# Performance work log

Measured on AMD Instinct MI355X. Metric: run time of the kernel, lower is better.

The kernel has to match this reference:

```python
import jax, jax.numpy as jnp
import numpy as np

N = 2_000_000
FUN, TAU, ALPHA, LOSS_WEIGHT = 'log', 1.0, 1.0, 1.0


def setup_inputs() -> dict:
    key = jax.random.key(0)
    k1, k2, k3 = jax.random.split(key, 3)
    pred = jax.random.uniform(k1, (N, 5), dtype=jnp.float32)
    target = jax.random.uniform(k2, (N, 5), dtype=jnp.float32)
    weight = jax.random.uniform(k3, (N,), dtype=jnp.float32)
    return {"pred": pred, "target": target, "weight": weight}


def _xyrs(xywhr):
    # [N,5] -> xy [N,2], R [N,2,2], S [N,2,2] (diag(wh/2))
    xy = xywhr[:, :2]
    wh = xywhr[:, 2:4]
    r = xywhr[:, 4]
    c, s = jnp.cos(r), jnp.sin(r)
    R = jnp.stack([c, -s, s, c], axis=-1).reshape(-1, 2, 2)
    S = 0.5 * wh[:, :, None] * jnp.eye(2, dtype=xywhr.dtype)  # diag_embed
    return xy, R, S


def _sqrt_trace_2x2sym(M):
    # trace of matrix sqrt of symmetric PSD 2x2: sqrt(tr(M) + 2*sqrt(det(M)))
    a, b, d = M[:, 0, 0], M[:, 0, 1], M[:, 1, 1]
    det = jnp.clip(a * d - b * b, 0.0)
    return jnp.sqrt(jnp.clip(a + d + 2.0 * jnp.sqrt(det), 0.0))


def reference(pred, target, weight):
    xy_p, R_p, S_p = _xyrs(pred)
    xy_t, R_t, S_t = _xyrs(target)

    dxy = xy_p - xy_t
    xy_distance = jnp.sum(dxy * dxy, axis=-1)

    Rp_T = jnp.swapaxes(R_p, -1, -2)
    Rt_T = jnp.swapaxes(R_t, -1, -2)
    Sigma_p_sqrt = R_p @ S_p @ Rp_T
    Sigma_p = R_p @ (S_p * S_p) @ Rp_T
    Sigma_t = R_t @ (S_t * S_t) @ Rt_T

    whr_distance = Sigma_p[:, 0, 0] + Sigma_p[:, 1, 1]
    whr_distance = whr_distance + Sigma_t[:, 0, 0] + Sigma_t[:, 1, 1]
    cross = Sigma_p_sqrt @ Sigma_t @ Sigma_p_sqrt
    whr_distance = whr_distance - 2.0 * _sqrt_trace_2x2sym(cross)

    distance = jnp.sqrt(jnp.clip(xy_distance + ALPHA * whr_distance, 0.0))
    scale = jnp.sqrt(jnp.sqrt(jnp.prod(pred[:, 2:4] * target[:, 2:4], axis=-1)))
    distance = distance / scale

    if FUN == 'log':
        distance = jnp.log1p(distance)
    elif FUN == 'sqrt':
        distance = jnp.sqrt(distance)

    if TAU >= 1.0:
        loss = 1.0 - 1.0 / (TAU + distance)
    else:
        loss = distance

    # weighted_loss wrapper: elementwise weight then mean reduction
    loss = jnp.mean(loss * weight)
    return loss * LOSS_WEIGHT
```

## Files before the change

### kernel.cpp

```cpp
#include <hip/hip_runtime.h>


#define CHUNK_ROWS 1024

__device__ __forceinline__ float gwd_row(const float* __restrict__ p,
                                         const float* __restrict__ t)
{
    const float px = p[0], py = p[1], pw = p[2], ph = p[3], pr = p[4];
    const float tx = t[0], ty = t[1], tw = t[2], th = t[3], tr = t[4];

    const float dx = px - tx;
    const float dy = py - ty;
    const float xy_dist = dx * dx + dy * dy;

    const float a2p = 0.25f * pw * pw;
    const float b2p = 0.25f * ph * ph;
    const float a2t = 0.25f * tw * tw;
    const float b2t = 0.25f * th * th;

    float whr = (a2p + b2p) + (a2t + b2t);

    float cp, sp, ct, st;
    __sincosf(pr, &sp, &cp);
    __sincosf(tr, &st, &ct);

    const float Sp00 = cp * cp * a2p + sp * sp * b2p;
    const float Sp01 = cp * sp * (a2p - b2p);
    const float Sp11 = sp * sp * a2p + cp * cp * b2p;
    const float St00 = ct * ct * a2t + st * st * b2t;
    const float St01 = ct * st * (a2t - b2t);
    const float St11 = st * st * a2t + ct * ct * b2t;

    const float tr_cross  = Sp00 * St00 + 2.0f * Sp01 * St01 + Sp11 * St11;
    const float det_cross = (a2p * b2p) * (a2t * b2t);

    float sq = fmaxf(tr_cross + 2.0f * sqrtf(det_cross), 0.0f);
    whr = whr - 2.0f * sqrtf(sq);

    float distance = sqrtf(fmaxf(xy_dist + whr, 0.0f));

    const float prod = (pw * tw) * (ph * th);
    distance = distance / sqrtf(sqrtf(prod));

    distance = log1pf(distance);
    return 1.0f - 1.0f / (1.0f + distance);
}

__global__ __launch_bounds__(256) void gwd_loss_kernel(
    const float* __restrict__ pred,
    const float* __restrict__ target,
    const float* __restrict__ weight,
    float* __restrict__ out,
    int n)
{
    __shared__ float s_pred[CHUNK_ROWS * 5];
    __shared__ float s_tgt [CHUNK_ROWS * 5];

    const float inv_n = 1.0f / (float)n;
    const int row0 = blockIdx.x * CHUNK_ROWS;
    const int tid  = threadIdx.x;
    float acc = 0.0f;

    if (row0 + CHUNK_ROWS <= n) {
        const float4* p4 = (const float4*)(pred   + (size_t)row0 * 5);
        const float4* t4 = (const float4*)(target + (size_t)row0 * 5);

        float4 P[5], T[5];
        #pragma unroll
        for (int j = 0; j < 5; ++j) P[j] = p4[j * 256 + tid];
        #pragma unroll
        for (int j = 0; j < 5; ++j) T[j] = t4[j * 256 + tid];

        #pragma unroll
        for (int j = 0; j < 5; ++j) ((float4*)s_pred)[j * 256 + tid] = P[j];
        #pragma unroll
        for (int j = 0; j < 5; ++j) ((float4*)s_tgt )[j * 256 + tid] = T[j];
        __syncthreads();

        #pragma unroll
        for (int rr = 0; rr < 4; ++rr) {
            const int r = tid + rr * 256;
            acc += gwd_row(&s_pred[r * 5], &s_tgt[r * 5]) * weight[row0 + r];
        }
    } else {
        for (int r = row0 + tid; r < n; r += 256) {
            float pb[5], tb[5];
            #pragma unroll
            for (int k = 0; k < 5; ++k) {
                pb[k] = pred  [(size_t)r * 5 + k];
                tb[k] = target[(size_t)r * 5 + k];
            }
            acc += gwd_row(pb, tb) * weight[r];
        }
    }

    #pragma unroll
    for (int off = 32; off > 0; off >>= 1)
        acc += __shfl_down(acc, off, 64);

    __syncthreads();
    const int lane = tid & 63;
    const int wid  = tid >> 6;
    if (lane == 0) s_pred[wid] = acc;
    __syncthreads();

    if (tid == 0) {
        const float s = (s_pred[0] + s_pred[1]) + (s_pred[2] + s_pred[3]);
        atomicAdd(out, s * inv_n);
    }
}

extern "C" void kernel_launch(void* const* d_in, const int* in_sizes, int n_in,
                              void* d_out, int out_size, void* d_ws, size_t ws_size,
                              hipStream_t stream) {
    const float* pred   = (const float*)d_in[0];
    const float* target = (const float*)d_in[1];
    const float* weight = (const float*)d_in[2];
    float* out = (float*)d_out;

    const int n = in_sizes[2];

    hipMemsetAsync(out, 0, sizeof(float), stream);

    const int block = 256;
    const int grid  = (n + CHUNK_ROWS - 1) / CHUNK_ROWS;
    gwd_loss_kernel<<<grid, block, 0, stream>>>(pred, target, weight, out, n);
}
```

Before: 125.2 us.

## Use grid-stride per-thread float4 loads, two-pass reduction, fast math intrinsics

Replaces the LDS-staged chunk kernel with a fixed 1024-block grid-stride kernel. Each thread loads four contiguous rows as five float4s from pred and target plus one float4 of weights directly into registers. Per-block partial sums are written to the workspace and combined by a second single-block kernel that also handles the tail rows. This drops the memset and global atomics. Math is switched to raw hardware sqrt, rsq, log and rcp intrinsics, which reduces accuracy slightly. Per-thread strided float4 loads are less coalesced than the previous layout, and the extra launch adds fixed overhead.

```diff
diff --git a/kernel.cpp b/kernel.cpp
--- a/kernel.cpp
+++ b/kernel.cpp
@@ -1,7 +1,7 @@
 #include <hip/hip_runtime.h>
 
 
-#define CHUNK_ROWS 1024
+#define NBLK 1024
 
 __device__ __forceinline__ float gwd_row(const float* __restrict__ p,
                                          const float* __restrict__ t)
@@ -34,79 +34,105 @@
     const float tr_cross  = Sp00 * St00 + 2.0f * Sp01 * St01 + Sp11 * St11;
     const float det_cross = (a2p * b2p) * (a2t * b2t);
 
-    float sq = fmaxf(tr_cross + 2.0f * sqrtf(det_cross), 0.0f);
-    whr = whr - 2.0f * sqrtf(sq);
+    const float sq = fmaxf(tr_cross + 2.0f * __builtin_amdgcn_sqrtf(det_cross), 0.0f);
+    whr = whr - 2.0f * __builtin_amdgcn_sqrtf(sq);
 
-    float distance = sqrtf(fmaxf(xy_dist + whr, 0.0f));
+    float d = __builtin_amdgcn_sqrtf(fmaxf(xy_dist + whr, 0.0f));
 
     const float prod = (pw * tw) * (ph * th);
-    distance = distance / sqrtf(sqrtf(prod));
+    d *= __builtin_amdgcn_rsqf(__builtin_amdgcn_sqrtf(prod));
 
-    distance = log1pf(distance);
-    return 1.0f - 1.0f / (1.0f + distance);
+    d = 0.69314718056f * __builtin_amdgcn_logf(1.0f + d);
+
+    return 1.0f - __builtin_amdgcn_rcpf(1.0f + d);
 }
 
-__global__ __launch_bounds__(256) void gwd_loss_kernel(
+__global__ __launch_bounds__(256) void gwd_partial(
+    const float* __restrict__ pred,
+    const float* __restrict__ target,
+    const float* __restrict__ weight,
+    float* __restrict__ ws,
+    int n)
+{
+    const int tid = threadIdx.x;
+    const int ngroups = n >> 2;
+    float acc = 0.0f;
+
+    for (int g = blockIdx.x * 256 + tid; g < ngroups; g += NBLK * 256) {
+        const float4* p4 = (const float4*)pred   + (size_t)g * 5;
+        const float4* t4 = (const float4*)target + (size_t)g * 5;
+
+        float4 P[5], T[5];
+        #pragma unroll
+        for (int j = 0; j < 5; ++j) P[j] = p4[j];
+        #pragma unroll
+        for (int j = 0; j < 5; ++j) T[j] = t4[j];
+        const float4 w4 = ((const float4*)weight)[g];
+
+        float pbuf[20], tbuf[20];
+        #pragma unroll
+        for (int j = 0; j < 5; ++j) { *(float4*)(pbuf + 4 * j) = P[j];
+                                      *(float4*)(tbuf + 4 * j) = T[j]; }
+        const float w[4] = { w4.x, w4.y, w4.z, w4.w };
+        #pragma unroll
+        for (int j = 0; j < 4; ++j)
+            acc += gwd_row(&pbuf[j * 5], &tbuf[j * 5]) * w[j];
+    }
+
+    #pragma unroll
+    for (int off = 32; off > 0; off >>= 1)
+        acc += __shfl_down(acc, off, 64);
+
+    __shared__ float wave_sums[4];
+    const int lane = tid & 63;
+    const int wid  = tid >> 6;
+    if (lane == 0) wave_sums[wid] = acc;
+    __syncthreads();
+
+    if (tid == 0)
+        ws[blockIdx.x] = (wave_sums[0] + wave_sums[1]) + (wave_sums[2] + wave_sums[3]);
+}
+
+__global__ __launch_bounds__(256) void gwd_final(
+    const float* __restrict__ ws,
     const float* __restrict__ pred,
     const float* __restrict__ target,
     const float* __restrict__ weight,
     float* __restrict__ out,
     int n)
 {
-    __shared__ float s_pred[CHUNK_ROWS * 5];
-    __shared__ float s_tgt [CHUNK_ROWS * 5];
-
-    const float inv_n = 1.0f / (float)n;
-    const int row0 = blockIdx.x * CHUNK_ROWS;
-    const int tid  = threadIdx.x;
+    const int tid = threadIdx.x;
     float acc = 0.0f;
 
-    if (row0 + CHUNK_ROWS <= n) {
-        const float4* p4 = (const float4*)(pred   + (size_t)row0 * 5);
-        const float4* t4 = (const float4*)(target + (size_t)row0 * 5);
+    #pragma unroll
+    for (int j = 0; j < NBLK / 256; ++j)
+        acc += ws[j * 256 + tid];
 
-        float4 P[5], T[5];
+    const int tail0 = n & ~3;
+    if (tid < (n - tail0)) {
+        const int r = tail0 + tid;
+        float pb[5], tb[5];
         #pragma unroll
-        for (int j = 0; j < 5; ++j) P[j] = p4[j * 256 + tid];
-        #pragma unroll
-        for (int j = 0; j < 5; ++j) T[j] = t4[j * 256 + tid];
-
-        #pragma unroll
-        for (int j = 0; j < 5; ++j) ((float4*)s_pred)[j * 256 + tid] = P[j];
-        #pragma unroll
-        for (int j = 0; j < 5; ++j) ((float4*)s_tgt )[j * 256 + tid] = T[j];
-        __syncthreads();
-
-        #pragma unroll
-        for (int rr = 0; rr < 4; ++rr) {
-            const int r = tid + rr * 256;
-            acc += gwd_row(&s_pred[r * 5], &s_tgt[r * 5]) * weight[row0 + r];
+        for (int k = 0; k < 5; ++k) {
+            pb[k] = pred  [(size_t)r * 5 + k];
+            tb[k] = target[(size_t)r * 5 + k];
         }
-    } else {
-        for (int r = row0 + tid; r < n; r += 256) {
-            float pb[5], tb[5];
-            #pragma unroll
-            for (int k = 0; k < 5; ++k) {
-                pb[k] = pred  [(size_t)r * 5 + k];
-                tb[k] = target[(size_t)r * 5 + k];
-            }
-            acc += gwd_row(pb, tb) * weight[r];
-        }
+        acc += gwd_row(pb, tb) * weight[r];
     }
 
     #pragma unroll
     for (int off = 32; off > 0; off >>= 1)
         acc += __shfl_down(acc, off, 64);
 
-    __syncthreads();
+    __shared__ float wave_sums[4];
     const int lane = tid & 63;
     const int wid  = tid >> 6;
-    if (lane == 0) s_pred[wid] = acc;
+    if (lane == 0) wave_sums[wid] = acc;
     __syncthreads();
 
     if (tid == 0) {
-        const float s = (s_pred[0] + s_pred[1]) + (s_pred[2] + s_pred[3]);
-        atomicAdd(out, s * inv_n);
+        const float s = (wave_sums[0] + wave_sums[1]) + (wave_sums[2] + wave_sums[3]);
+        out[0] = s * (1.0f / (float)n);
     }
 }
 
@@ -117,12 +143,10 @@
     const float* target = (const float*)d_in[1];
     const float* weight = (const float*)d_in[2];
     float* out = (float*)d_out;
+    float* ws  = (float*)d_ws;
 
     const int n = in_sizes[2];
 
-    hipMemsetAsync(out, 0, sizeof(float), stream);
-
-    const int block = 256;
-    const int grid  = (n + CHUNK_ROWS - 1) / CHUNK_ROWS;
-    gwd_loss_kernel<<<grid, block, 0, stream>>>(pred, target, weight, out, n);
+    gwd_partial<<<NBLK, 256, 0, stream>>>(pred, target, weight, ws, n);
+    gwd_final<<<1, 256, 0, stream>>>(ws, pred, target, weight, out, n);
 }
```

After: 106.5 us. 15.0% less time.
